# Kernel tuning notes

Measured on AMD Instinct MI355X. Metric: run time of the kernel, lower is better.

## Reference

```python
import jax, jax.numpy as jnp
import numpy as np

B, Q, K = 4, 2048, 2048
D_IN = 1024
H, D_ATN, D_V, D_OUT = 16, 64, 64, 1024
NEG = -1e10


def setup_inputs() -> dict:
    key = jax.random.key(0)
    ks = jax.random.split(key, 8)
    queries = jax.random.normal(ks[0], (B, Q, D_IN), dtype=jnp.float32)
    keys = jax.random.normal(ks[1], (B, K, D_IN), dtype=jnp.float32)
    values = jax.random.normal(ks[2], (B, K, D_IN), dtype=jnp.float32)
    mask = jax.random.randint(ks[3], (B, Q, K), 0, 2, dtype=jnp.int32)
    s = 1.0 / np.sqrt(D_IN)
    Wq = jax.random.normal(ks[4], (D_IN, D_ATN * H), dtype=jnp.float32) * s
    Wk = jax.random.normal(ks[5], (D_IN, D_ATN * H), dtype=jnp.float32) * s
    Wv = jax.random.normal(ks[6], (D_IN, D_V * H), dtype=jnp.float32) * s
    Wo = jax.random.normal(ks[7], (H * D_V, D_OUT), dtype=jnp.float32) * (1.0 / np.sqrt(H * D_V))
    return {"queries": queries, "keys": keys, "values": values, "mask": mask,
            "Wq": Wq, "Wk": Wk, "Wv": Wv, "Wo": Wo}


def reference(queries, keys, values, mask, Wq, Wk, Wv, Wo):
    # project and split heads as in torch: view(B, S, -1, num_heads) -> head axis LAST
    qs = (queries @ Wq).reshape(B, Q, D_ATN, H)  # [b, i, d, h]
    ks = (keys @ Wk).reshape(B, K, D_ATN, H)     # [b, o, d, h]
    vs = (values @ Wv).reshape(B, K, D_V, H)     # [b, o, d, h]
    scale = jnp.sqrt(jnp.asarray(D_ATN, dtype=qs.dtype))
    w = jnp.einsum('bidh,bodh->bioh', qs, ks) / scale  # [b, i, o, h]
    w = jnp.where(mask[..., None] == 0, NEG, w)
    w = jax.nn.softmax(w, axis=-2)  # softmax over keys (o) axis
    mha = jnp.einsum('bioh,bodh->bidh', w, vs).reshape(B, Q, D_V * H)
    return mha @ Wo
```

## Files before the change

kernel.cpp:

```cpp
#include <hip/hip_runtime.h>


typedef __bf16 bf16x8 __attribute__((ext_vector_type(8)));
typedef __bf16 bf16x4 __attribute__((ext_vector_type(4)));
typedef float f32x4 __attribute__((ext_vector_type(4)));

__device__ __forceinline__ unsigned short f2bf(float f) {
  union { float f; unsigned u; } x; x.f = f;
  unsigned r = x.u + 0x7fffu + ((x.u >> 16) & 1u);
  return (unsigned short)(r >> 16);
}

__device__ __forceinline__ float exp2fast(float x) {
#if __has_builtin(__builtin_amdgcn_exp2f)
  return __builtin_amdgcn_exp2f(x);
#else
  return exp2f(x);
#endif
}

__device__ __forceinline__ f32x4 mfma16(bf16x8 a, bf16x8 b, f32x4 c) {
  return __builtin_amdgcn_mfma_f32_16x16x32_bf16(a, b, c, 0, 0, 0);
}

__device__ __forceinline__ void gl16(const void* g, void* l) {
  __builtin_amdgcn_global_load_lds(
      (const __attribute__((address_space(1))) unsigned int*)g,
      (__attribute__((address_space(3))) unsigned int*)l, 16, 0, 0);
}

__device__ __forceinline__ unsigned cvtpk(float lo, float hi) {
  unsigned r;
  asm("v_cvt_pk_bf16_f32 %0, %1, %2" : "=v"(r) : "v"(lo), "v"(hi));
  return r;
}
__device__ __forceinline__ void swap32(unsigned &a, unsigned &b) {
  asm("v_permlane32_swap_b32 %0, %1" : "+v"(a), "+v"(b));
}
__device__ __forceinline__ void swap16(unsigned &a, unsigned &b) {
  asm("v_permlane16_swap_b32 %0, %1" : "+v"(a), "+v"(b));
}

__device__ __forceinline__ int permf(int x) { return ((x & 15) << 6) | (x >> 4); }
__device__ __forceinline__ int ipermf(int x) { return ((x & 63) << 4) | (x >> 6); }

__global__ __launch_bounds__(256) void wtrans_k(const float* __restrict__ W0,
                                                const float* __restrict__ W1,
                                                const float* __restrict__ W2,
                                                const float* __restrict__ W3,
                                                unsigned short* __restrict__ T0,
                                                unsigned short* __restrict__ T1,
                                                unsigned short* __restrict__ T2,
                                                unsigned short* __restrict__ T3) {
  const int z = blockIdx.z;
  const float* W = z == 0 ? W0 : z == 1 ? W1 : z == 2 ? W2 : W3;
  unsigned short* T = z == 0 ? T0 : z == 1 ? T1 : z == 2 ? T2 : T3;
  __shared__ float t[32][33];
  int n0 = blockIdx.x * 32, k0 = blockIdx.y * 32;
  int tx = threadIdx.x, ty = threadIdx.y;
#pragma unroll
  for (int r = 0; r < 32; r += 8) {
    int srow = (z == 3) ? ipermf(k0 + ty + r) : (k0 + ty + r);
    t[ty + r][tx] = W[(long)srow * 1024 + n0 + tx];
  }
  __syncthreads();
#pragma unroll
  for (int r = 0; r < 32; r += 8) {
    int drow = (z < 3) ? permf(n0 + ty + r) : (n0 + ty + r);
    T[(long)drow * 1024 + k0 + tx] = f2bf(t[tx][ty + r]);
  }
}

__global__ __launch_bounds__(256) void maskbits_k(const int* __restrict__ m,
                                                  unsigned long long* __restrict__ mb) {
  long i = (long)blockIdx.x * 256 + threadIdx.x;
  unsigned long long b = __ballot(m[i] != 0);
  if ((threadIdx.x & 63) == 0) mb[i >> 6] = b;
}

__global__ __launch_bounds__(256) void cvt_k(const float* __restrict__ q,
                                             const float* __restrict__ k,
                                             const float* __restrict__ v,
                                             unsigned short* __restrict__ o0,
                                             unsigned short* __restrict__ o1,
                                             unsigned short* __restrict__ o2) {
  const float* in = blockIdx.y == 0 ? q : blockIdx.y == 1 ? k : v;
  unsigned short* out = blockIdx.y == 0 ? o0 : blockIdx.y == 1 ? o1 : o2;
  long i = ((long)blockIdx.x * 256 + threadIdx.x) * 8;
  float4 a = *(const float4*)(in + i);
  float4 b = *(const float4*)(in + i + 4);
  union { bf16x8 v8; uint4 u; } o;
  o.v8[0] = (__bf16)a.x; o.v8[1] = (__bf16)a.y; o.v8[2] = (__bf16)a.z; o.v8[3] = (__bf16)a.w;
  o.v8[4] = (__bf16)b.x; o.v8[5] = (__bf16)b.y; o.v8[6] = (__bf16)b.z; o.v8[7] = (__bf16)b.w;
  *(uint4*)(out + i) = o.u;
}

template <int OUTMODE>
__global__ __launch_bounds__(256, 2) void gemm2_k(const unsigned short* __restrict__ A,
                                                  const unsigned short* __restrict__ Bt,
                                                  void* __restrict__ Out, float scale) {
  __shared__ __align__(16) char lds[2][32768];
  const int t = threadIdx.x, lane = t & 63, wv = t >> 6;
  const int wm = wv >> 1, wn = wv & 1;
  const int id = blockIdx.x;
  const int logical = (id & 7) * 64 + (id >> 3);
  const int i0 = (logical >> 3) * 128, n0 = (logical & 7) * 128;
  const int lr = lane & 15, lg = lane >> 4;

  long aoff[4], boff[4];
#pragma unroll
  for (int j = 0; j < 4; ++j) {
    int c = j * 256 + t, r = c >> 3, kc = (c & 7) ^ (r & 7);
    aoff[j] = ((long)(i0 + r) << 10) + kc * 8;
    boff[j] = ((long)(n0 + r) << 10) + kc * 8;
  }

  f32x4 zero = {0.f, 0.f, 0.f, 0.f};
  f32x4 acc[4][4];
#pragma unroll
  for (int mt = 0; mt < 4; ++mt)
#pragma unroll
    for (int nt = 0; nt < 4; ++nt) acc[mt][nt] = zero;

#pragma unroll
  for (int j = 0; j < 4; ++j) {
    gl16(A + aoff[j], &lds[0][j * 4096 + wv * 1024]);
    gl16(Bt + boff[j], &lds[0][16384 + j * 4096 + wv * 1024]);
  }
  __syncthreads();

  for (int ks = 0; ks < 16; ++ks) {
    const int cur = ks & 1;
    if (ks + 1 < 16) {
      const unsigned short* Ak = A + (ks + 1) * 64;
      const unsigned short* Bk = Bt + (ks + 1) * 64;
#pragma unroll
      for (int j = 0; j < 4; ++j) {
        gl16(Ak + aoff[j], &lds[cur ^ 1][j * 4096 + wv * 1024]);
        gl16(Bk + boff[j], &lds[cur ^ 1][16384 + j * 4096 + wv * 1024]);
      }
    }
    const char* Ab = &lds[cur][0];
    const char* Bb = &lds[cur][16384];
    bf16x8 af[2][4], bfr[2][4];
#pragma unroll
    for (int mt = 0; mt < 4; ++mt) {
      int r = wm * 64 + mt * 16 + lr;
      int sw = (r & 7) << 4;
      af[0][mt] = *(const bf16x8*)(Ab + r * 128 + ((lg * 16) ^ sw));
      af[1][mt] = *(const bf16x8*)(Ab + r * 128 + ((64 + lg * 16) ^ sw));
    }
#pragma unroll
    for (int nt = 0; nt < 4; ++nt) {
      int r = wn * 64 + nt * 16 + lr;
      int sw = (r & 7) << 4;
      bfr[0][nt] = *(const bf16x8*)(Bb + r * 128 + ((lg * 16) ^ sw));
      bfr[1][nt] = *(const bf16x8*)(Bb + r * 128 + ((64 + lg * 16) ^ sw));
    }
#pragma unroll
    for (int h2 = 0; h2 < 2; ++h2)
#pragma unroll
      for (int mt = 0; mt < 4; ++mt)
#pragma unroll
        for (int nt = 0; nt < 4; ++nt)
          acc[mt][nt] = mfma16(af[h2][mt], bfr[h2][nt], acc[mt][nt]);
    __syncthreads();
  }

  if (OUTMODE == 2) {
    float* O = (float*)Out;
#pragma unroll
    for (int mt = 0; mt < 4; ++mt)
#pragma unroll
      for (int nt = 0; nt < 4; ++nt)
#pragma unroll
        for (int r = 0; r < 4; ++r) {
          int row = i0 + wm * 64 + mt * 16 + lg * 4 + r;
          int col = n0 + wn * 64 + nt * 16 + lr;
          O[(long)row * 1024 + col] = acc[mt][nt][r];
        }
  } else if (OUTMODE == 0) {
    unsigned short* O = (unsigned short*)Out;
#pragma unroll
    for (int mt = 0; mt < 4; ++mt)
#pragma unroll
      for (int nt = 0; nt < 4; ++nt) {
        int col = n0 + wn * 64 + nt * 16 + lr;
        int h = col >> 6, d = col & 63;
#pragma unroll
        for (int r = 0; r < 4; ++r) {
          int row = i0 + wm * 64 + mt * 16 + lg * 4 + r;
          int b = row >> 11, s = row & 2047;
          O[(((long)(b * 16 + h) * 2048 + s) << 6) + d] = f2bf(acc[mt][nt][r] * scale);
        }
      }
  } else if (OUTMODE == 3) {
    char* O = (char*)Out;
#pragma unroll
    for (int mt = 0; mt < 4; ++mt)
#pragma unroll
      for (int nt = 0; nt < 4; ++nt) {
        int col = n0 + wn * 64 + nt * 16 + lr;
        int h = col >> 6, d = col & 63;
#pragma unroll
        for (int r = 0; r < 4; ++r) {
          int row = i0 + wm * 64 + mt * 16 + lg * 4 + r;
          int b = row >> 11, s = row & 2047;
          int bh = b * 16 + h, ts = s >> 6, key = s & 63;
          long byte = ((long)(bh * 32 + ts) << 13) + key * 128 + ((d * 2) ^ ((key & 7) << 4));
          unsigned short bv = f2bf(acc[mt][nt][r]);
          *(unsigned short*)(O + byte) = bv;
        }
      }
  } else {
    char* O = (char*)Out;
#pragma unroll
    for (int mt = 0; mt < 4; ++mt)
#pragma unroll
      for (int nt = 0; nt < 4; ++nt) {
        int col = n0 + wn * 64 + nt * 16 + lr;
        int h = col >> 6, d = col & 63;
        int row0 = i0 + wm * 64 + mt * 16 + lg * 4;
        int b = row0 >> 11, s0 = row0 & 2047;
        int bh = b * 16 + h, ts = s0 >> 6, key0 = s0 & 63;
        ushort4 w;
        w.x = f2bf(acc[mt][nt][0]); w.y = f2bf(acc[mt][nt][1]);
        w.z = f2bf(acc[mt][nt][2]); w.w = f2bf(acc[mt][nt][3]);
        long byte = ((long)(bh * 32 + ts) << 13) + d * 128 + ((key0 * 2) ^ ((d & 7) << 4));
        *(ushort4*)(O + byte) = w;
      }
  }
}

__global__ __launch_bounds__(256, 2) void attn_k(const unsigned short* __restrict__ Qh,
                                                 const unsigned short* __restrict__ Kh,
                                                 const unsigned short* __restrict__ Vt,
                                                 const unsigned long long* __restrict__ MB,
                                                 unsigned short* __restrict__ Mha) {
  __shared__ __align__(16) char kv[2][16384];
  const int t = threadIdx.x, lane = t & 63, wv = t >> 6;
  const int id = blockIdx.x;
  const int logical = (id & 7) * 64 + (id >> 3);
  const int bh = logical >> 3, qt = logical & 7;
  const int b = bh >> 4, h = bh & 15;
  const int i0 = qt * 256 + wv * 64;
  const int lr = lane & 15, lg = lane >> 4;

  const unsigned short* Qp = Qh + ((long)bh * 2048 + i0) * 64;
  const char* Kg = (const char*)Kh + ((long)bh << 18);
  const char* Vg = (const char*)Vt + ((long)bh << 18);
  const unsigned long long* mrow[4];
#pragma unroll
  for (int g = 0; g < 4; ++g) mrow[g] = MB + ((long)b * 2048 + i0 + g * 16 + lr) * 32;
  const int swz = (lr & 7) << 4;
  const int goff = wv * 2048 + lane * 16;
  const int loff = wv * 2048;

  bf16x8 qf0[4], qf1[4];
#pragma unroll
  for (int g = 0; g < 4; ++g) {
    qf0[g] = *(const bf16x8*)(Qp + (g * 16 + lr) * 64 + lg * 8);
    qf1[g] = *(const bf16x8*)(Qp + (g * 16 + lr) * 64 + 32 + lg * 8);
  }

  bf16x8 ones;
#pragma unroll
  for (int i = 0; i < 8; ++i) ones[i] = (__bf16)1.0f;

  f32x4 zero = {0.f, 0.f, 0.f, 0.f};
  f32x4 oa[4][4];
#pragma unroll
  for (int g = 0; g < 4; ++g)
#pragma unroll
    for (int dt = 0; dt < 4; ++dt) oa[g][dt] = zero;
  float l[4] = {0.f, 0.f, 0.f, 0.f};

  {
    char* dst = &kv[0][0];
    gl16(Kg + goff, dst + loff);
    gl16(Kg + goff + 1024, dst + loff + 1024);
    gl16(Vg + goff, dst + 8192 + loff);
    gl16(Vg + goff + 1024, dst + 8192 + loff + 1024);
  }
  __syncthreads();

  for (int ts = 0; ts < 32; ++ts) {
    const int cur = ts & 1;
    if (ts + 1 < 32) {
      const char* kg = Kg + ((long)(ts + 1) << 13);
      const char* vg = Vg + ((long)(ts + 1) << 13);
      char* dst = &kv[cur ^ 1][0];
      gl16(kg + goff, dst + loff);
      gl16(kg + goff + 1024, dst + loff + 1024);
      gl16(vg + goff, dst + 8192 + loff);
      gl16(vg + goff + 1024, dst + 8192 + loff + 1024);
    }
    unsigned milo[4], mihi[4];
#pragma unroll
    for (int g = 0; g < 4; ++g) {
      unsigned long long ms = mrow[g][ts] >> (4 * lg);
      milo[g] = ~(unsigned)ms;
      mihi[g] = ~(unsigned)(ms >> 32);
    }

    const char* Kb = &kv[cur][0];
    const char* Vb = &kv[cur][8192];
    f32x4 sv[4][4];
#pragma unroll
    for (int nt = 0; nt < 4; ++nt) {
      int key = nt * 16 + lr;
      int ksz = (key & 7) << 4;
      bf16x8 kf0 = *(const bf16x8*)(Kb + key * 128 + ((lg * 16) ^ ksz));
      bf16x8 kf1 = *(const bf16x8*)(Kb + key * 128 + ((lg * 16 + 64) ^ ksz));
#pragma unroll
      for (int g = 0; g < 4; ++g) {
        unsigned w = (nt < 2) ? milo[g] : mihi[g];
        f32x4 z;
#pragma unroll
        for (int r = 0; r < 4; ++r) {
          int mb = ((int)(w << (31 - ((nt & 1) * 16 + r)))) >> 31;
          z[r] = __int_as_float(mb & 0xC6EA6000);
        }
        sv[g][nt] = mfma16(kf1, qf1[g], mfma16(kf0, qf0[g], z));
      }
    }
#pragma unroll
    for (int g = 0; g < 4; ++g)
#pragma unroll
      for (int nt = 0; nt < 4; ++nt)
#pragma unroll
        for (int r = 0; r < 4; ++r) sv[g][nt][r] = exp2fast(sv[g][nt][r]);
    union pu { unsigned w[4]; bf16x8 v; };
    pu pa0[4], pa1[4];
#pragma unroll
    for (int g = 0; g < 4; ++g) {
      unsigned u00 = cvtpk(sv[g][0][0], sv[g][0][1]), u01 = cvtpk(sv[g][0][2], sv[g][0][3]);
      unsigned u10 = cvtpk(sv[g][1][0], sv[g][1][1]), u11 = cvtpk(sv[g][1][2], sv[g][1][3]);
      unsigned u20 = cvtpk(sv[g][2][0], sv[g][2][1]), u21 = cvtpk(sv[g][2][2], sv[g][2][3]);
      unsigned u30 = cvtpk(sv[g][3][0], sv[g][3][1]), u31 = cvtpk(sv[g][3][2], sv[g][3][3]);
      swap32(u00, u10); swap16(u00, u10);
      swap32(u01, u11); swap16(u01, u11);
      pa0[g].w[0] = u00; pa0[g].w[1] = u01; pa0[g].w[2] = u10; pa0[g].w[3] = u11;
      swap32(u20, u30); swap16(u20, u30);
      swap32(u21, u31); swap16(u21, u31);
      pa1[g].w[0] = u20; pa1[g].w[1] = u21; pa1[g].w[2] = u30; pa1[g].w[3] = u31;
    }
#pragma unroll
    for (int g = 0; g < 4; ++g) {
      f32x4 rs = mfma16(ones, pa1[g].v, mfma16(ones, pa0[g].v, zero));
      l[g] += rs[0];
    }
#pragma unroll
    for (int dt = 0; dt < 4; ++dt) {
      int d = dt * 16 + lr;
      int vsz = (d & 7) << 4;
      bf16x8 vf0 = *(const bf16x8*)(Vb + d * 128 + ((lg * 16) ^ vsz));
      bf16x8 vf1 = *(const bf16x8*)(Vb + d * 128 + ((lg * 16 + 64) ^ vsz));
#pragma unroll
      for (int g = 0; g < 4; ++g)
        oa[g][dt] = mfma16(vf1, pa1[g].v, mfma16(vf0, pa0[g].v, oa[g][dt]));
    }
    __syncthreads();
  }
  char* scr = &kv[0][0] + wv * 8192;
#pragma unroll
  for (int g = 0; g < 4; ++g) {
    float inv = 1.f / l[g];
#pragma unroll
    for (int dt = 0; dt < 4; ++dt) {
      bf16x4 w;
#pragma unroll
      for (int r = 0; r < 4; ++r) w[r] = (__bf16)(oa[g][dt][r] * inv);
      *(bf16x4*)(scr + g * 2048 + lr * 128 + ((dt * 32 + lg * 8) ^ swz)) = w;
    }
  }
#pragma unroll
  for (int g = 0; g < 4; ++g) {
    unsigned short* Op = Mha + ((long)b * 2048 + i0 + g * 16 + lr) * 1024 + h * 64 + lg * 16;
    int b0 = g * 2048 + lr * 128 + ((lg * 32) ^ swz);
    int b1 = g * 2048 + lr * 128 + ((lg * 32 + 16) ^ swz);
    uint4 lo = *(const uint4*)(scr + b0), hi = *(const uint4*)(scr + b1);
    *(uint4*)(Op) = lo;
    *(uint4*)(Op + 8) = hi;
  }
}

extern "C" void kernel_launch(void* const* d_in, const int* in_sizes, int n_in,
                              void* d_out, int out_size, void* d_ws, size_t ws_size,
                              hipStream_t stream) {
  const float* q = (const float*)d_in[0];
  const float* k = (const float*)d_in[1];
  const float* v = (const float*)d_in[2];
  const int* mask = (const int*)d_in[3];
  const float* Wq = (const float*)d_in[4];
  const float* Wk = (const float*)d_in[5];
  const float* Wv = (const float*)d_in[6];
  const float* Wo = (const float*)d_in[7];
  (void)in_sizes; (void)n_in; (void)out_size; (void)ws_size;

  char* ws = (char*)d_ws;
  unsigned short* Wqt = (unsigned short*)(ws + (0ul << 20));
  unsigned short* Wkt = (unsigned short*)(ws + (2ul << 20));
  unsigned short* Wvt = (unsigned short*)(ws + (4ul << 20));
  unsigned short* Wot = (unsigned short*)(ws + (6ul << 20));
  unsigned long long* MBp = (unsigned long long*)(ws + (8ul << 20));
  unsigned short* Qh  = (unsigned short*)(ws + (10ul << 20));
  unsigned short* Kh  = (unsigned short*)(ws + (26ul << 20));
  unsigned short* Vt  = (unsigned short*)(ws + (42ul << 20));
  unsigned short* Mha = (unsigned short*)(ws + (58ul << 20));
  unsigned short* X1 = Mha, *X2 = Qh, *X3 = Kh;

  wtrans_k<<<dim3(32, 32, 4), dim3(32, 8), 0, stream>>>(Wq, Wk, Wv, Wo, Wqt, Wkt, Wvt, Wot);
  maskbits_k<<<65536, 256, 0, stream>>>(mask, MBp);
  cvt_k<<<dim3(4096, 3), 256, 0, stream>>>(q, k, v, X1, X2, X3);

  gemm2_k<4><<<512, 256, 0, stream>>>(X3, Wvt, Vt, 1.0f);
  gemm2_k<3><<<512, 256, 0, stream>>>(X2, Wkt, Kh, 1.0f);
  gemm2_k<0><<<512, 256, 0, stream>>>(X1, Wqt, Qh, 0.125f * 1.44269504f);

  attn_k<<<512, 256, 0, stream>>>(Qh, Kh, Vt, MBp, Mha);

  gemm2_k<2><<<512, 256, 0, stream>>>(Mha, Wot, d_out, 1.0f);
}
```

Measured before the change: 252.4 us.

## Merge prep kernels and double the attention KV tile per sync

The three preprocessing kernels (weight transpose, mask bit-packing, bf16 conversion) are merged into one launch that dispatches on block index, removing two launch gaps. The attention kernel now stages two 64-key tiles per buffer (32KB per stage), which halves the number of barriers and prefetch points in the K/V loop. It also raises wave priority around the PV MFMA section via s_setprio. The larger LDS footprint (64KB per block) may limit occupancy to fewer blocks per CU.

```diff
diff --git a/kernel.cpp b/kernel.cpp
--- a/kernel.cpp
+++ b/kernel.cpp
@@ -44,55 +44,59 @@
 __device__ __forceinline__ int permf(int x) { return ((x & 15) << 6) | (x >> 4); }
 __device__ __forceinline__ int ipermf(int x) { return ((x & 63) << 4) | (x >> 6); }
 
-__global__ __launch_bounds__(256) void wtrans_k(const float* __restrict__ W0,
-                                                const float* __restrict__ W1,
-                                                const float* __restrict__ W2,
-                                                const float* __restrict__ W3,
-                                                unsigned short* __restrict__ T0,
-                                                unsigned short* __restrict__ T1,
-                                                unsigned short* __restrict__ T2,
-                                                unsigned short* __restrict__ T3) {
-  const int z = blockIdx.z;
-  const float* W = z == 0 ? W0 : z == 1 ? W1 : z == 2 ? W2 : W3;
-  unsigned short* T = z == 0 ? T0 : z == 1 ? T1 : z == 2 ? T2 : T3;
-  __shared__ float t[32][33];
-  int n0 = blockIdx.x * 32, k0 = blockIdx.y * 32;
-  int tx = threadIdx.x, ty = threadIdx.y;
-#pragma unroll
-  for (int r = 0; r < 32; r += 8) {
-    int srow = (z == 3) ? ipermf(k0 + ty + r) : (k0 + ty + r);
-    t[ty + r][tx] = W[(long)srow * 1024 + n0 + tx];
-  }
-  __syncthreads();
-#pragma unroll
-  for (int r = 0; r < 32; r += 8) {
-    int drow = (z < 3) ? permf(n0 + ty + r) : (n0 + ty + r);
-    T[(long)drow * 1024 + k0 + tx] = f2bf(t[tx][ty + r]);
-  }
-}
-
-__global__ __launch_bounds__(256) void maskbits_k(const int* __restrict__ m,
-                                                  unsigned long long* __restrict__ mb) {
-  long i = (long)blockIdx.x * 256 + threadIdx.x;
-  unsigned long long b = __ballot(m[i] != 0);
-  if ((threadIdx.x & 63) == 0) mb[i >> 6] = b;
-}
-
-__global__ __launch_bounds__(256) void cvt_k(const float* __restrict__ q,
-                                             const float* __restrict__ k,
-                                             const float* __restrict__ v,
-                                             unsigned short* __restrict__ o0,
-                                             unsigned short* __restrict__ o1,
-                                             unsigned short* __restrict__ o2) {
-  const float* in = blockIdx.y == 0 ? q : blockIdx.y == 1 ? k : v;
-  unsigned short* out = blockIdx.y == 0 ? o0 : blockIdx.y == 1 ? o1 : o2;
-  long i = ((long)blockIdx.x * 256 + threadIdx.x) * 8;
-  float4 a = *(const float4*)(in + i);
-  float4 b = *(const float4*)(in + i + 4);
-  union { bf16x8 v8; uint4 u; } o;
-  o.v8[0] = (__bf16)a.x; o.v8[1] = (__bf16)a.y; o.v8[2] = (__bf16)a.z; o.v8[3] = (__bf16)a.w;
-  o.v8[4] = (__bf16)b.x; o.v8[5] = (__bf16)b.y; o.v8[6] = (__bf16)b.z; o.v8[7] = (__bf16)b.w;
-  *(uint4*)(out + i) = o.u;
+__global__ __launch_bounds__(256) void prep_k(const float* __restrict__ q,
+                                              const float* __restrict__ k,
+                                              const float* __restrict__ v,
+                                              const int* __restrict__ mask,
+                                              const float* __restrict__ W0,
+                                              const float* __restrict__ W1,
+                                              const float* __restrict__ W2,
+                                              const float* __restrict__ W3,
+                                              unsigned short* __restrict__ T0,
+                                              unsigned short* __restrict__ T1,
+                                              unsigned short* __restrict__ T2,
+                                              unsigned short* __restrict__ T3,
+                                              unsigned long long* __restrict__ mb,
+                                              unsigned short* __restrict__ o0,
+                                              unsigned short* __restrict__ o1,
+                                              unsigned short* __restrict__ o2) {
+  __shared__ float sh[32][33];
+  const int id = blockIdx.x, t = threadIdx.x;
+  if (id < 65536) {
+    long i = (long)id * 256 + t;
+    unsigned long long b = __ballot(mask[i] != 0);
+    if ((t & 63) == 0) mb[i >> 6] = b;
+  } else if (id < 77824) {
+    int id2 = id - 65536;
+    int which = id2 >> 12, x = id2 & 4095;
+    const float* in = which == 0 ? q : which == 1 ? k : v;
+    unsigned short* out = which == 0 ? o0 : which == 1 ? o1 : o2;
+    long i = ((long)x * 256 + t) * 8;
+    float4 a = *(const float4*)(in + i);
+    float4 b4 = *(const float4*)(in + i + 4);
+    union { bf16x8 v8; uint4 u; } o;
+    o.v8[0] = (__bf16)a.x; o.v8[1] = (__bf16)a.y; o.v8[2] = (__bf16)a.z; o.v8[3] = (__bf16)a.w;
+    o.v8[4] = (__bf16)b4.x; o.v8[5] = (__bf16)b4.y; o.v8[6] = (__bf16)b4.z; o.v8[7] = (__bf16)b4.w;
+    *(uint4*)(out + i) = o.u;
+  } else {
+    int id3 = id - 77824;
+    int z = id3 >> 10, rem = id3 & 1023;
+    int n0 = (rem & 31) * 32, k0 = (rem >> 5) * 32;
+    const float* W = z == 0 ? W0 : z == 1 ? W1 : z == 2 ? W2 : W3;
+    unsigned short* T = z == 0 ? T0 : z == 1 ? T1 : z == 2 ? T2 : T3;
+    int tx = t & 31, ty = t >> 5;
+#pragma unroll
+    for (int r = 0; r < 32; r += 8) {
+      int srow = (z == 3) ? ipermf(k0 + ty + r) : (k0 + ty + r);
+      sh[ty + r][tx] = W[(long)srow * 1024 + n0 + tx];
+    }
+    __syncthreads();
+#pragma unroll
+    for (int r = 0; r < 32; r += 8) {
+      int drow = (z < 3) ? permf(n0 + ty + r) : (n0 + ty + r);
+      T[(long)drow * 1024 + k0 + tx] = f2bf(sh[tx][ty + r]);
+    }
+  }
 }
 
 template <int OUTMODE>
@@ -237,7 +241,7 @@
                                                  const unsigned short* __restrict__ Vt,
                                                  const unsigned long long* __restrict__ MB,
                                                  unsigned short* __restrict__ Mha) {
-  __shared__ __align__(16) char kv[2][16384];
+  __shared__ __align__(16) char kv[2][32768];
   const int t = threadIdx.x, lane = t & 63, wv = t >> 6;
   const int id = blockIdx.x;
   const int logical = (id & 7) * 64 + (id >> 3);
@@ -275,36 +279,28 @@
     for (int dt = 0; dt < 4; ++dt) oa[g][dt] = zero;
   float l[4] = {0.f, 0.f, 0.f, 0.f};
 
-  {
-    char* dst = &kv[0][0];
-    gl16(Kg + goff, dst + loff);
-    gl16(Kg + goff + 1024, dst + loff + 1024);
-    gl16(Vg + goff, dst + 8192 + loff);
-    gl16(Vg + goff + 1024, dst + 8192 + loff + 1024);
-  }
-  __syncthreads();
-
-  for (int ts = 0; ts < 32; ++ts) {
-    const int cur = ts & 1;
-    if (ts + 1 < 32) {
-      const char* kg = Kg + ((long)(ts + 1) << 13);
-      const char* vg = Vg + ((long)(ts + 1) << 13);
-      char* dst = &kv[cur ^ 1][0];
-      gl16(kg + goff, dst + loff);
-      gl16(kg + goff + 1024, dst + loff + 1024);
-      gl16(vg + goff, dst + 8192 + loff);
-      gl16(vg + goff + 1024, dst + 8192 + loff + 1024);
-    }
+  auto stage2 = [&](int tp) {
+    const char* kg = Kg + ((long)tp << 14);
+    const char* vg = Vg + ((long)tp << 14);
+    char* dst = &kv[tp & 1][0];
+    gl16(kg + goff, dst + loff);
+    gl16(kg + goff + 1024, dst + loff + 1024);
+    gl16(vg + goff, dst + 8192 + loff);
+    gl16(vg + goff + 1024, dst + 8192 + loff + 1024);
+    gl16(kg + 8192 + goff, dst + 16384 + loff);
+    gl16(kg + 8192 + goff + 1024, dst + 16384 + loff + 1024);
+    gl16(vg + 8192 + goff, dst + 24576 + loff);
+    gl16(vg + 8192 + goff + 1024, dst + 24576 + loff + 1024);
+  };
+
+  auto proc = [&](int ts, const char* Kb, const char* Vb) {
     unsigned milo[4], mihi[4];
 #pragma unroll
     for (int g = 0; g < 4; ++g) {
-      unsigned long long ms = mrow[g][ts] >> (4 * lg);
-      milo[g] = ~(unsigned)ms;
-      mihi[g] = ~(unsigned)(ms >> 32);
-    }
-
-    const char* Kb = &kv[cur][0];
-    const char* Vb = &kv[cur][8192];
+      unsigned long long msv = mrow[g][ts] >> (4 * lg);
+      milo[g] = ~(unsigned)msv;
+      mihi[g] = ~(unsigned)(msv >> 32);
+    }
     f32x4 sv[4][4];
 #pragma unroll
     for (int nt = 0; nt < 4; ++nt) {
@@ -350,6 +346,7 @@
       f32x4 rs = mfma16(ones, pa1[g].v, mfma16(ones, pa0[g].v, zero));
       l[g] += rs[0];
     }
+    __builtin_amdgcn_s_setprio(1);
 #pragma unroll
     for (int dt = 0; dt < 4; ++dt) {
       int d = dt * 16 + lr;
@@ -360,8 +357,21 @@
       for (int g = 0; g < 4; ++g)
         oa[g][dt] = mfma16(vf1, pa1[g].v, mfma16(vf0, pa0[g].v, oa[g][dt]));
     }
+    __builtin_amdgcn_s_setprio(0);
+  };
+
+  stage2(0);
+  __syncthreads();
+
+  for (int tp = 0; tp < 16; ++tp) {
+    const int cur = tp & 1;
+    if (tp + 1 < 16) stage2(tp + 1);
+    const char* base = &kv[cur][0];
+    proc(2 * tp, base, base + 8192);
+    proc(2 * tp + 1, base + 16384, base + 24576);
     __syncthreads();
   }
+
   char* scr = &kv[0][0] + wv * 8192;
 #pragma unroll
   for (int g = 0; g < 4; ++g) {
@@ -410,9 +420,8 @@
   unsigned short* Mha = (unsigned short*)(ws + (58ul << 20));
   unsigned short* X1 = Mha, *X2 = Qh, *X3 = Kh;
 
-  wtrans_k<<<dim3(32, 32, 4), dim3(32, 8), 0, stream>>>(Wq, Wk, Wv, Wo, Wqt, Wkt, Wvt, Wot);
-  maskbits_k<<<65536, 256, 0, stream>>>(mask, MBp);
-  cvt_k<<<dim3(4096, 3), 256, 0, stream>>>(q, k, v, X1, X2, X3);
+  prep_k<<<81920, 256, 0, stream>>>(q, k, v, mask, Wq, Wk, Wv, Wo,
+                                    Wqt, Wkt, Wvt, Wot, MBp, X1, X2, X3);
 
   gemm2_k<4><<<512, 256, 0, stream>>>(X3, Wvt, Vt, 1.0f);
   gemm2_k<3><<<512, 256, 0, stream>>>(X2, Wkt, Kh, 1.0f);
```

New measurement: 245.6 us. 2.7% less time.
